# Optimization experiments

Measured on AMD Instinct MI355X. Metric: run time of the kernel, lower is better.

## Reference

```python
import jax, jax.numpy as jnp
import numpy as np

N = 20000      # nodes
E = 320000     # directed edges (before self-loops)
IN, HID, HEADS, OUT = 512, 256, 4, 256
NEG_SLOPE = 0.2  # PyG GATConv default


def setup_inputs() -> dict:
    key = jax.random.key(0)
    ks = jax.random.split(key, 10)
    x = jax.random.normal(ks[0], (N, IN), jnp.float32)
    edge_index = jax.random.randint(ks[1], (2, E), 0, N, jnp.int32)
    W1 = jax.random.normal(ks[2], (IN, HEADS * HID), jnp.float32) / np.sqrt(IN).astype(np.float32)
    att_src1 = jax.random.normal(ks[3], (HEADS, HID), jnp.float32) * 0.1
    att_dst1 = jax.random.normal(ks[4], (HEADS, HID), jnp.float32) * 0.1
    b1 = jnp.zeros((HEADS * HID,), jnp.float32)
    W2 = jax.random.normal(ks[5], (HEADS * HID, OUT), jnp.float32) / np.sqrt(HEADS * HID).astype(np.float32)
    att_src2 = jax.random.normal(ks[6], (1, OUT), jnp.float32) * 0.1
    att_dst2 = jax.random.normal(ks[7], (1, OUT), jnp.float32) * 0.1
    b2 = jnp.zeros((OUT,), jnp.float32)
    return {"x": x, "edge_index": edge_index, "W1": W1, "att_src1": att_src1,
            "att_dst1": att_dst1, "b1": b1, "W2": W2, "att_src2": att_src2,
            "att_dst2": att_dst2, "b2": b2}


def _segment_softmax(logits, seg, num_segments):
    # softmax over edges grouped by destination node (per head)
    m = jax.ops.segment_max(logits, seg, num_segments=num_segments)
    ex = jnp.exp(logits - m[seg])
    s = jax.ops.segment_sum(ex, seg, num_segments=num_segments)
    return ex / (s[seg] + 1e-16)


def _gat_conv(x, src, dst, W, att_src, att_dst, bias, heads, ch, num_nodes, concat):
    # PyG GATConv: h = W x (per head); alpha_e = softmax_dst(LeakyReLU(a_s.h_src + a_d.h_dst))
    h = (x @ W).reshape(num_nodes, heads, ch)          # [N,H,C]
    a_s = (h * att_src).sum(-1)                        # [N,H]
    a_d = (h * att_dst).sum(-1)                        # [N,H]
    logits = jax.nn.leaky_relu(a_s[src] + a_d[dst], NEG_SLOPE)   # [E,H]
    alpha = _segment_softmax(logits, dst, num_nodes)             # [E,H]
    msg = h[src] * alpha[:, :, None]                             # [E,H,C]
    out = jax.ops.segment_sum(msg, dst, num_segments=num_nodes)  # [N,H,C]
    out = out.reshape(num_nodes, heads * ch) if concat else out.mean(axis=1)
    return out + bias


def reference(x, edge_index, W1, att_src1, att_dst1, b1, W2, att_src2, att_dst2, b2):
    # add self-loops (PyG default add_self_loops=True)
    loop = jnp.arange(N, dtype=edge_index.dtype)
    src = jnp.concatenate([edge_index[0], loop])
    dst = jnp.concatenate([edge_index[1], loop])
    h = jax.nn.elu(_gat_conv(x, src, dst, W1, att_src1, att_dst1, b1, HEADS, HID, N, True))
    return _gat_conv(h, src, dst, W2, att_src2, att_dst2, b2, 1, OUT, N, False)
```

## Files before the change

### kernel.cpp

```cpp
#include <hip/hip_runtime.h>
#include <hip/hip_bf16.h>
#include <cfloat>
#include <math.h>

#define N_NODES 20000
#define M_PAD   20096
#define N_EDGES 320000
#define TOT_E   (N_EDGES + N_NODES)
#define IN_F    512
#define HID     256
#define HEADS   4
#define OUT_F   256
#define H1DIM   (HEADS * HID)
#define NEG_SLOPE 0.2f

typedef __attribute__((ext_vector_type(8))) __bf16 bf16x8;
typedef __attribute__((ext_vector_type(4))) __bf16 bf16x4;
typedef __attribute__((ext_vector_type(4))) float f32x4;

__device__ __forceinline__ float lrelu(float x) { return x >= 0.f ? x : NEG_SLOPE * x; }

__global__ void k_count(const int* __restrict__ ei, int* __restrict__ deg) {
  int e = blockIdx.x * 256 + threadIdx.x;
  if (e >= TOT_E) return;
  int dst = (e < N_EDGES) ? ei[N_EDGES + e] : (e - N_EDGES);
  atomicAdd(&deg[dst], 1);
}

__global__ void k_scan(const int* __restrict__ deg, int* __restrict__ off) {
  __shared__ int part[256];
  int tid = threadIdx.x;
  const int chunk = (N_NODES + 255) / 256;
  int s0 = tid * chunk;
  int s1 = s0 + chunk; if (s1 > N_NODES) s1 = N_NODES; if (s0 > N_NODES) s0 = N_NODES;
  int s = 0;
  for (int i = s0; i < s1; ++i) s += deg[i];
  part[tid] = s;
  __syncthreads();
  for (int d = 1; d < 256; d <<= 1) {
    int v = (tid >= d) ? part[tid - d] : 0;
    __syncthreads();
    part[tid] += v;
    __syncthreads();
  }
  int run = (tid == 0) ? 0 : part[tid - 1];
  for (int i = s0; i < s1; ++i) { off[i] = run; run += deg[i]; }
  if (tid == 255) off[N_NODES] = run;
}

__global__ void k_fill(const int* __restrict__ ei, const int* __restrict__ off,
                       int* __restrict__ cur, int* __restrict__ csr_src) {
  int e = blockIdx.x * 256 + threadIdx.x;
  if (e >= TOT_E) return;
  int src, dst;
  if (e < N_EDGES) { src = ei[e]; dst = ei[N_EDGES + e]; }
  else             { src = dst = e - N_EDGES; }
  int pos = atomicAdd(&cur[dst], 1);
  csr_src[off[dst] + pos] = src;
}

__global__ void k_f2b(const float* __restrict__ in, __bf16* __restrict__ out, int n4) {
  int i = blockIdx.x * 256 + threadIdx.x;
  if (i >= n4) return;
  float4 v = ((const float4*)in)[i];
  bf16x4 o = { (__bf16)v.x, (__bf16)v.y, (__bf16)v.z, (__bf16)v.w };
  ((bf16x4*)out)[i] = o;
}

__global__ void k_tr_f2b(const float* __restrict__ in, __bf16* __restrict__ out,
                         int R, int Cc) {
  __shared__ float tile[32][33];
  int c0 = blockIdx.x * 32, r0 = blockIdx.y * 32;
  int tx = threadIdx.x & 31, ty = threadIdx.x >> 5;
  for (int rr = ty; rr < 32; rr += 8)
    tile[rr][tx] = in[(size_t)(r0 + rr) * Cc + c0 + tx];
  __syncthreads();
  for (int rr = ty; rr < 32; rr += 8)
    out[(size_t)(c0 + rr) * R + r0 + tx] = (__bf16)tile[tx][rr];
}

__global__ __launch_bounds__(256) void k_gemm_bf16(
    const __bf16* __restrict__ A,
    const __bf16* __restrict__ Bt,
    __bf16* __restrict__ Cb,
    int M, int N, int K)
{
  __shared__ char lds[32768];
  char* As = lds;
  char* Bs = lds + 16384;

  const int t = threadIdx.x;
  const int lane = t & 63;
  const int wid = t >> 6;
  const int wm = wid >> 1, wn = wid & 1;
  const int row0 = blockIdx.y * 128;
  const int col0 = blockIdx.x * 128;

  f32x4 acc[4][4];
#pragma unroll
  for (int i = 0; i < 4; ++i)
#pragma unroll
    for (int j = 0; j < 4; ++j) acc[i][j] = (f32x4){0.f, 0.f, 0.f, 0.f};

  for (int k0 = 0; k0 < K; k0 += 64) {
#pragma unroll
    for (int i = 0; i < 4; ++i) {
      int j = i * 256 + t;
      int r = j >> 3;
      int cc = (j & 7) ^ (r & 7);
      const __bf16* gp = A + (size_t)(row0 + r) * K + k0 + cc * 8;
      __builtin_amdgcn_global_load_lds(
          (const __attribute__((address_space(1))) void*)gp,
          (__attribute__((address_space(3))) void*)(As + j * 16), 16, 0, 0);
    }
#pragma unroll
    for (int i = 0; i < 4; ++i) {
      int j = i * 256 + t;
      int r = j >> 3;
      int cc = (j & 7) ^ (r & 7);
      const __bf16* gp = Bt + (size_t)(col0 + r) * K + k0 + cc * 8;
      __builtin_amdgcn_global_load_lds(
          (const __attribute__((address_space(1))) void*)gp,
          (__attribute__((address_space(3))) void*)(Bs + j * 16), 16, 0, 0);
    }
    __syncthreads();

#pragma unroll
    for (int ks = 0; ks < 2; ++ks) {
      bf16x8 af[4], bfr[4];
#pragma unroll
      for (int i = 0; i < 4; ++i) {
        int rA = wm * 64 + i * 16 + (lane & 15);
        int chA = (ks * 4 + (lane >> 4)) ^ (rA & 7);
        af[i] = *(const bf16x8*)(As + rA * 128 + chA * 16);
        int rB = wn * 64 + i * 16 + (lane & 15);
        int chB = (ks * 4 + (lane >> 4)) ^ (rB & 7);
        bfr[i] = *(const bf16x8*)(Bs + rB * 128 + chB * 16);
      }
#pragma unroll
      for (int i = 0; i < 4; ++i)
#pragma unroll
        for (int jn = 0; jn < 4; ++jn)
          acc[i][jn] = __builtin_amdgcn_mfma_f32_16x16x32_bf16(
              af[i], bfr[jn], acc[i][jn], 0, 0, 0);
    }
    __syncthreads();
  }

#pragma unroll
  for (int i = 0; i < 4; ++i) {
    int growb = row0 + wm * 64 + i * 16 + (lane >> 4) * 4;
#pragma unroll
    for (int jn = 0; jn < 4; ++jn) {
      int gcol = col0 + wn * 64 + jn * 16 + (lane & 15);
#pragma unroll
      for (int r = 0; r < 4; ++r) {
        int grow = growb + r;
        if (grow < M) Cb[(size_t)grow * N + gcol] = (__bf16)acc[i][jn][r];
      }
    }
  }
}

__global__ void k_attn1(const __bf16* __restrict__ h1b, const float* __restrict__ att_s,
                        const float* __restrict__ att_d, float* __restrict__ as,
                        float* __restrict__ ad) {
  int n = blockIdx.x;
  int t = threadIdx.x;
  int head = t >> 6, lane = t & 63;
  bf16x4 hv = *(const bf16x4*)(h1b + (size_t)n * H1DIM + t * 4);
  float4 sv = *(const float4*)(att_s + t * 4);
  float4 dv = *(const float4*)(att_d + t * 4);
  float h0 = (float)hv[0], h1 = (float)hv[1], h2 = (float)hv[2], h3 = (float)hv[3];
  float ss = h0 * sv.x + h1 * sv.y + h2 * sv.z + h3 * sv.w;
  float sd = h0 * dv.x + h1 * dv.y + h2 * dv.z + h3 * dv.w;
#pragma unroll
  for (int d = 32; d; d >>= 1) { ss += __shfl_xor(ss, d); sd += __shfl_xor(sd, d); }
  if (lane == 0) { as[n * HEADS + head] = ss; ad[n * HEADS + head] = sd; }
}

__global__ void k_attn2(const __bf16* __restrict__ h2b, const float* __restrict__ att_s,
                        const float* __restrict__ att_d, float* __restrict__ as,
                        float* __restrict__ ad) {
  int n = blockIdx.x;
  int lane = threadIdx.x;
  bf16x4 hv = *(const bf16x4*)(h2b + (size_t)n * OUT_F + lane * 4);
  float4 sv = *(const float4*)(att_s + lane * 4);
  float4 dv = *(const float4*)(att_d + lane * 4);
  float h0 = (float)hv[0], h1 = (float)hv[1], h2 = (float)hv[2], h3 = (float)hv[3];
  float ss = h0 * sv.x + h1 * sv.y + h2 * sv.z + h3 * sv.w;
  float sd = h0 * dv.x + h1 * dv.y + h2 * dv.z + h3 * dv.w;
#pragma unroll
  for (int d = 32; d; d >>= 1) { ss += __shfl_xor(ss, d); sd += __shfl_xor(sd, d); }
  if (lane == 0) { as[n] = ss; ad[n] = sd; }
}

__global__ void k_w1(const int* __restrict__ off, const int* __restrict__ csr,
                     const float* __restrict__ as, const float* __restrict__ ad,
                     float* __restrict__ wn, float* __restrict__ inv) {
  int n = blockIdx.x;
  int lane = threadIdx.x;
  int beg = off[n], end = off[n + 1];
  float4 adv = *(const float4*)&ad[n * 4];
  float p0 = 0.f, p1 = 0.f, p2 = 0.f, p3 = 0.f;
  for (int p = beg + lane; p < end; p += 64) {
    int s = csr[p];
    float4 av = *(const float4*)&as[s * 4];
    float w0 = __expf(lrelu(av.x + adv.x));
    float w1 = __expf(lrelu(av.y + adv.y));
    float w2 = __expf(lrelu(av.z + adv.z));
    float w3 = __expf(lrelu(av.w + adv.w));
    p0 += w0; p1 += w1; p2 += w2; p3 += w3;
    float4 wv = {w0, w1, w2, w3};
    *(float4*)&wn[(size_t)p * 4] = wv;
  }
#pragma unroll
  for (int d = 32; d; d >>= 1) {
    p0 += __shfl_xor(p0, d); p1 += __shfl_xor(p1, d);
    p2 += __shfl_xor(p2, d); p3 += __shfl_xor(p3, d);
  }
  if (lane == 0) {
    float4 iv = {1.f / (p0 + 1e-16f), 1.f / (p1 + 1e-16f),
                 1.f / (p2 + 1e-16f), 1.f / (p3 + 1e-16f)};
    *(float4*)&inv[n * 4] = iv;
  }
}

__global__ void k_w2(const int* __restrict__ off, const int* __restrict__ csr,
                     const float* __restrict__ as, const float* __restrict__ ad,
                     float* __restrict__ wn, float* __restrict__ inv) {
  int n = blockIdx.x;
  int lane = threadIdx.x;
  int beg = off[n], end = off[n + 1];
  float adv = ad[n];
  float ps = 0.f;
  for (int p = beg + lane; p < end; p += 64) {
    int s = csr[p];
    float w = __expf(lrelu(as[s] + adv));
    wn[p] = w;
    ps += w;
  }
#pragma unroll
  for (int d = 32; d; d >>= 1) ps += __shfl_xor(ps, d);
  if (lane == 0) inv[n] = 1.f / (ps + 1e-16f);
}

__global__ __launch_bounds__(256) void k_gather1(
    const int* __restrict__ off, const int* __restrict__ csr,
    const __bf16* __restrict__ h1b, const float* __restrict__ wn,
    const float* __restrict__ inv, const float* __restrict__ b1,
    __bf16* __restrict__ heluB) {
  int bid = blockIdx.x;
  int slice = bid & 7;
  int grp = bid >> 3;
  int wid = threadIdx.x >> 6, lane = threadIdx.x & 63;
  int n = grp * 4 + wid;
  int cb = slice * 128;
  int head = slice >> 1;
  int sub = lane >> 4, cg = lane & 15;
  int beg = off[n], end = off[n + 1];

  float acc[8] = {0.f, 0.f, 0.f, 0.f, 0.f, 0.f, 0.f, 0.f};
  const __bf16* hb = h1b + cb + cg * 8;
#pragma unroll 2
  for (int p = beg; p < end; p += 4) {
    int e = p + sub;
    float w = 0.f; int s = 0;
    if (e < end) { s = csr[e]; w = wn[(size_t)e * 4 + head]; }
    bf16x8 hv = *(const bf16x8*)(hb + (size_t)s * H1DIM);
#pragma unroll
    for (int k = 0; k < 8; ++k) acc[k] += w * (float)hv[k];
  }
#pragma unroll
  for (int k = 0; k < 8; ++k) {
    acc[k] += __shfl_xor(acc[k], 16);
    acc[k] += __shfl_xor(acc[k], 32);
  }
  if (sub == 0) {
    float iv = inv[n * 4 + head];
    float4 b0 = *(const float4*)(b1 + cb + cg * 8);
    float4 b1v = *(const float4*)(b1 + cb + cg * 8 + 4);
    float bb[8] = {b0.x, b0.y, b0.z, b0.w, b1v.x, b1v.y, b1v.z, b1v.w};
    bf16x8 o;
#pragma unroll
    for (int k = 0; k < 8; ++k) {
      float v = acc[k] * iv + bb[k];
      v = v > 0.f ? v : expm1f(v);
      o[k] = (__bf16)v;
    }
    *(bf16x8*)(heluB + (size_t)n * H1DIM + cb + cg * 8) = o;
  }
}

__global__ __launch_bounds__(256) void k_gather2(
    const int* __restrict__ off, const int* __restrict__ csr,
    const __bf16* __restrict__ h2b, const float* __restrict__ wn,
    const float* __restrict__ inv, const float* __restrict__ b2,
    float* __restrict__ out) {
  int bid = blockIdx.x;
  int slice = bid & 3;
  int grp = bid >> 2;
  int wid = threadIdx.x >> 6, lane = threadIdx.x & 63;
  int n = grp * 4 + wid;
  int cb = slice * 64;
  int sub = lane >> 3, cg = lane & 7;
  int beg = off[n], end = off[n + 1];

  float acc[8] = {0.f, 0.f, 0.f, 0.f, 0.f, 0.f, 0.f, 0.f};
  const __bf16* hb = h2b + cb + cg * 8;
#pragma unroll 2
  for (int p = beg; p < end; p += 8) {
    int e = p + sub;
    float w = 0.f; int s = 0;
    if (e < end) { s = csr[e]; w = wn[e]; }
    bf16x8 hv = *(const bf16x8*)(hb + (size_t)s * OUT_F);
#pragma unroll
    for (int k = 0; k < 8; ++k) acc[k] += w * (float)hv[k];
  }
#pragma unroll
  for (int k = 0; k < 8; ++k) {
    acc[k] += __shfl_xor(acc[k], 8);
    acc[k] += __shfl_xor(acc[k], 16);
    acc[k] += __shfl_xor(acc[k], 32);
  }
  if (sub == 0) {
    float iv = inv[n];
    float4 b0 = *(const float4*)(b2 + cb + cg * 8);
    float4 b1v = *(const float4*)(b2 + cb + cg * 8 + 4);
    float* op = out + (size_t)n * OUT_F + cb + cg * 8;
    float4 o0 = {acc[0] * iv + b0.x, acc[1] * iv + b0.y,
                 acc[2] * iv + b0.z, acc[3] * iv + b0.w};
    float4 o1 = {acc[4] * iv + b1v.x, acc[5] * iv + b1v.y,
                 acc[6] * iv + b1v.z, acc[7] * iv + b1v.w};
    *(float4*)op = o0;
    *(float4*)(op + 4) = o1;
  }
}

extern "C" void kernel_launch(void* const* d_in, const int* in_sizes, int n_in,
                              void* d_out, int out_size, void* d_ws, size_t ws_size,
                              hipStream_t stream) {
  const float* x      = (const float*)d_in[0];
  const int*   ei     = (const int*)d_in[1];
  const float* W1     = (const float*)d_in[2];
  const float* att_s1 = (const float*)d_in[3];
  const float* att_d1 = (const float*)d_in[4];
  const float* b1     = (const float*)d_in[5];
  const float* W2     = (const float*)d_in[6];
  const float* att_s2 = (const float*)d_in[7];
  const float* att_d2 = (const float*)d_in[8];
  const float* b2     = (const float*)d_in[9];
  float* out = (float*)d_out;

  char* w = (char*)d_ws;
  auto alloc = [&](size_t bytes) {
    char* p = w;
    w += (bytes + 255) & ~(size_t)255;
    return p;
  };
  int*    deg   = (int*)alloc((size_t)N_NODES * 4);
  int*    off   = (int*)alloc((size_t)(N_NODES + 1) * 4);
  int*    cur   = (int*)alloc((size_t)N_NODES * 4);
  int*    csr   = (int*)alloc((size_t)TOT_E * 4);
  float*  as1   = (float*)alloc((size_t)N_NODES * HEADS * 4);
  float*  ad1   = (float*)alloc((size_t)N_NODES * HEADS * 4);
  float*  as2   = (float*)alloc((size_t)N_NODES * 4);
  float*  ad2   = (float*)alloc((size_t)N_NODES * 4);
  float*  wn1   = (float*)alloc((size_t)TOT_E * HEADS * 4);
  float*  inv1  = (float*)alloc((size_t)N_NODES * HEADS * 4);
  float*  wn2   = (float*)alloc((size_t)TOT_E * 4);
  float*  inv2  = (float*)alloc((size_t)N_NODES * 4);
  __bf16* xb    = (__bf16*)alloc((size_t)M_PAD * IN_F * 2);
  __bf16* w1t   = (__bf16*)alloc((size_t)H1DIM * IN_F * 2);
  __bf16* w2t   = (__bf16*)alloc((size_t)OUT_F * H1DIM * 2);
  __bf16* h1b   = (__bf16*)alloc((size_t)M_PAD * H1DIM * 2);
  __bf16* heluB = (__bf16*)alloc((size_t)M_PAD * H1DIM * 2);
  __bf16* h2b   = (__bf16*)alloc((size_t)M_PAD * OUT_F * 2);
  if ((size_t)(w - (char*)d_ws) > ws_size) return;

  hipMemsetAsync(deg, 0, (size_t)N_NODES * 4, stream);
  hipMemsetAsync(cur, 0, (size_t)N_NODES * 4, stream);

  k_count<<<(TOT_E + 255) / 256, 256, 0, stream>>>(ei, deg);
  k_scan<<<1, 256, 0, stream>>>(deg, off);
  k_fill<<<(TOT_E + 255) / 256, 256, 0, stream>>>(ei, off, cur, csr);

  int n4 = N_NODES * IN_F / 4;
  k_f2b<<<(n4 + 255) / 256, 256, 0, stream>>>(x, xb, n4);
  k_tr_f2b<<<dim3(H1DIM / 32, IN_F / 32), 256, 0, stream>>>(W1, w1t, IN_F, H1DIM);
  k_tr_f2b<<<dim3(OUT_F / 32, H1DIM / 32), 256, 0, stream>>>(W2, w2t, H1DIM, OUT_F);

  k_gemm_bf16<<<dim3(H1DIM / 128, M_PAD / 128), 256, 0, stream>>>(
      xb, w1t, h1b, N_NODES, H1DIM, IN_F);
  k_attn1<<<N_NODES, 256, 0, stream>>>(h1b, att_s1, att_d1, as1, ad1);
  k_w1<<<N_NODES, 64, 0, stream>>>(off, csr, as1, ad1, wn1, inv1);
  k_gather1<<<(N_NODES / 4) * 8, 256, 0, stream>>>(off, csr, h1b, wn1, inv1, b1, heluB);

  k_gemm_bf16<<<dim3(OUT_F / 128, M_PAD / 128), 256, 0, stream>>>(
      heluB, w2t, h2b, N_NODES, OUT_F, H1DIM);
  k_attn2<<<N_NODES, 64, 0, stream>>>(h2b, att_s2, att_d2, as2, ad2);
  k_w2<<<N_NODES, 64, 0, stream>>>(off, csr, as2, ad2, wn2, inv2);
  k_gather2<<<(N_NODES / 4) * 4, 256, 0, stream>>>(off, csr, h2b, wn2, inv2, b2, out);
}
```

Before: 324.0 us.

## Map multiple nodes per wave in gather kernels, drop cross-lane reductions

Both gather kernels now give each 16-lane (layer 1) or 8-lane (layer 2) lane group its own destination node. Each group walks that node's edges serially up to the wave's maximum degree, instead of splitting one node's edges across sub-groups and reducing with shuffles. This removes the shuffle reductions and the single-writer epilogue. It also uses bit-shift bf16 unpacking and a cheaper ELU. Edge arrays are padded and zeroed so overrun reads past the max-degree stay in bounds. The tradeoff is that lanes with small degree idle while the wave waits on its highest-degree node.

```diff
diff --git a/kernel.cpp b/kernel.cpp
--- a/kernel.cpp
+++ b/kernel.cpp
@@ -7,6 +7,7 @@
 #define M_PAD   20096
 #define N_EDGES 320000
 #define TOT_E   (N_EDGES + N_NODES)
+#define EPAD    512
 #define IN_F    512
 #define HID     256
 #define HEADS   4
@@ -19,6 +20,7 @@
 typedef __attribute__((ext_vector_type(4))) float f32x4;
 
 __device__ __forceinline__ float lrelu(float x) { return x >= 0.f ? x : NEG_SLOPE * x; }
+__device__ __forceinline__ float elu_lite(float x) { return x > 0.f ? x : __expf(x) - 1.f; }
 
 __global__ void k_count(const int* __restrict__ ei, int* __restrict__ deg) {
   int e = blockIdx.x * 256 + threadIdx.x;
@@ -252,44 +254,47 @@
     __bf16* __restrict__ heluB) {
   int bid = blockIdx.x;
   int slice = bid & 7;
-  int grp = bid >> 3;
-  int wid = threadIdx.x >> 6, lane = threadIdx.x & 63;
-  int n = grp * 4 + wid;
+  int head = slice >> 1;
   int cb = slice * 128;
-  int head = slice >> 1;
-  int sub = lane >> 4, cg = lane & 15;
+  int w = threadIdx.x >> 6, lane = threadIdx.x & 63;
+  int g = lane >> 4;
+  int cg = lane & 15;
+  int n = (bid >> 3) * 16 + w * 4 + g;
   int beg = off[n], end = off[n + 1];
+  int deg = end - beg;
+  int itmax = deg;
+  itmax = max(itmax, __shfl_xor(itmax, 16));
+  itmax = max(itmax, __shfl_xor(itmax, 32));
 
   float acc[8] = {0.f, 0.f, 0.f, 0.f, 0.f, 0.f, 0.f, 0.f};
   const __bf16* hb = h1b + cb + cg * 8;
 #pragma unroll 2
-  for (int p = beg; p < end; p += 4) {
-    int e = p + sub;
-    float w = 0.f; int s = 0;
-    if (e < end) { s = csr[e]; w = wn[(size_t)e * 4 + head]; }
-    bf16x8 hv = *(const bf16x8*)(hb + (size_t)s * H1DIM);
-#pragma unroll
-    for (int k = 0; k < 8; ++k) acc[k] += w * (float)hv[k];
-  }
+  for (int i = 0; i < itmax; ++i) {
+    int e = beg + i;
+    int s = csr[e];
+    float wv = (i < deg) ? wn[(size_t)e * 4 + head] : 0.f;
+    uint4 u = *(const uint4*)(hb + (size_t)s * H1DIM);
+    acc[0] = fmaf(wv, __uint_as_float(u.x << 16), acc[0]);
+    acc[1] = fmaf(wv, __uint_as_float(u.x & 0xffff0000u), acc[1]);
+    acc[2] = fmaf(wv, __uint_as_float(u.y << 16), acc[2]);
+    acc[3] = fmaf(wv, __uint_as_float(u.y & 0xffff0000u), acc[3]);
+    acc[4] = fmaf(wv, __uint_as_float(u.z << 16), acc[4]);
+    acc[5] = fmaf(wv, __uint_as_float(u.z & 0xffff0000u), acc[5]);
+    acc[6] = fmaf(wv, __uint_as_float(u.w << 16), acc[6]);
+    acc[7] = fmaf(wv, __uint_as_float(u.w & 0xffff0000u), acc[7]);
+  }
+
+  float iv = inv[n * 4 + head];
+  float4 bv0 = *(const float4*)(b1 + cb + cg * 8);
+  float4 bv1 = *(const float4*)(b1 + cb + cg * 8 + 4);
+  float bb[8] = {bv0.x, bv0.y, bv0.z, bv0.w, bv1.x, bv1.y, bv1.z, bv1.w};
+  bf16x8 o;
 #pragma unroll
   for (int k = 0; k < 8; ++k) {
-    acc[k] += __shfl_xor(acc[k], 16);
-    acc[k] += __shfl_xor(acc[k], 32);
-  }
-  if (sub == 0) {
-    float iv = inv[n * 4 + head];
-    float4 b0 = *(const float4*)(b1 + cb + cg * 8);
-    float4 b1v = *(const float4*)(b1 + cb + cg * 8 + 4);
-    float bb[8] = {b0.x, b0.y, b0.z, b0.w, b1v.x, b1v.y, b1v.z, b1v.w};
-    bf16x8 o;
-#pragma unroll
-    for (int k = 0; k < 8; ++k) {
-      float v = acc[k] * iv + bb[k];
-      v = v > 0.f ? v : expm1f(v);
-      o[k] = (__bf16)v;
-    }
-    *(bf16x8*)(heluB + (size_t)n * H1DIM + cb + cg * 8) = o;
-  }
+    float v = acc[k] * iv + bb[k];
+    o[k] = (__bf16)elu_lite(v);
+  }
+  *(bf16x8*)(heluB + (size_t)n * H1DIM + cb + cg * 8) = o;
 }
 
 __global__ __launch_bounds__(256) void k_gather2(
@@ -299,42 +304,46 @@
     float* __restrict__ out) {
   int bid = blockIdx.x;
   int slice = bid & 3;
-  int grp = bid >> 2;
-  int wid = threadIdx.x >> 6, lane = threadIdx.x & 63;
-  int n = grp * 4 + wid;
   int cb = slice * 64;
-  int sub = lane >> 3, cg = lane & 7;
+  int w = threadIdx.x >> 6, lane = threadIdx.x & 63;
+  int g = lane >> 3;
+  int cg = lane & 7;
+  int n = (bid >> 2) * 32 + w * 8 + g;
   int beg = off[n], end = off[n + 1];
+  int deg = end - beg;
+  int itmax = deg;
+  itmax = max(itmax, __shfl_xor(itmax, 8));
+  itmax = max(itmax, __shfl_xor(itmax, 16));
+  itmax = max(itmax, __shfl_xor(itmax, 32));
 
   float acc[8] = {0.f, 0.f, 0.f, 0.f, 0.f, 0.f, 0.f, 0.f};
   const __bf16* hb = h2b + cb + cg * 8;
 #pragma unroll 2
-  for (int p = beg; p < end; p += 8) {
-    int e = p + sub;
-    float w = 0.f; int s = 0;
-    if (e < end) { s = csr[e]; w = wn[e]; }
-    bf16x8 hv = *(const bf16x8*)(hb + (size_t)s * OUT_F);
-#pragma unroll
-    for (int k = 0; k < 8; ++k) acc[k] += w * (float)hv[k];
-  }
-#pragma unroll
-  for (int k = 0; k < 8; ++k) {
-    acc[k] += __shfl_xor(acc[k], 8);
-    acc[k] += __shfl_xor(acc[k], 16);
-    acc[k] += __shfl_xor(acc[k], 32);
-  }
-  if (sub == 0) {
-    float iv = inv[n];
-    float4 b0 = *(const float4*)(b2 + cb + cg * 8);
-    float4 b1v = *(const float4*)(b2 + cb + cg * 8 + 4);
-    float* op = out + (size_t)n * OUT_F + cb + cg * 8;
-    float4 o0 = {acc[0] * iv + b0.x, acc[1] * iv + b0.y,
-                 acc[2] * iv + b0.z, acc[3] * iv + b0.w};
-    float4 o1 = {acc[4] * iv + b1v.x, acc[5] * iv + b1v.y,
-                 acc[6] * iv + b1v.z, acc[7] * iv + b1v.w};
-    *(float4*)op = o0;
-    *(float4*)(op + 4) = o1;
-  }
+  for (int i = 0; i < itmax; ++i) {
+    int e = beg + i;
+    int s = csr[e];
+    float wv = (i < deg) ? wn[e] : 0.f;
+    uint4 u = *(const uint4*)(hb + (size_t)s * OUT_F);
+    acc[0] = fmaf(wv, __uint_as_float(u.x << 16), acc[0]);
+    acc[1] = fmaf(wv, __uint_as_float(u.x & 0xffff0000u), acc[1]);
+    acc[2] = fmaf(wv, __uint_as_float(u.y << 16), acc[2]);
+    acc[3] = fmaf(wv, __uint_as_float(u.y & 0xffff0000u), acc[3]);
+    acc[4] = fmaf(wv, __uint_as_float(u.z << 16), acc[4]);
+    acc[5] = fmaf(wv, __uint_as_float(u.z & 0xffff0000u), acc[5]);
+    acc[6] = fmaf(wv, __uint_as_float(u.w << 16), acc[6]);
+    acc[7] = fmaf(wv, __uint_as_float(u.w & 0xffff0000u), acc[7]);
+  }
+
+  float iv = inv[n];
+  float4 bv0 = *(const float4*)(b2 + cb + cg * 8);
+  float4 bv1 = *(const float4*)(b2 + cb + cg * 8 + 4);
+  float* op = out + (size_t)n * OUT_F + cb + cg * 8;
+  float4 o0 = {acc[0] * iv + bv0.x, acc[1] * iv + bv0.y,
+               acc[2] * iv + bv0.z, acc[3] * iv + bv0.w};
+  float4 o1 = {acc[4] * iv + bv1.x, acc[5] * iv + bv1.y,
+               acc[6] * iv + bv1.z, acc[7] * iv + bv1.w};
+  *(float4*)op = o0;
+  *(float4*)(op + 4) = o1;
 }
 
 extern "C" void kernel_launch(void* const* d_in, const int* in_sizes, int n_in,
@@ -361,14 +370,14 @@
   int*    deg   = (int*)alloc((size_t)N_NODES * 4);
   int*    off   = (int*)alloc((size_t)(N_NODES + 1) * 4);
   int*    cur   = (int*)alloc((size_t)N_NODES * 4);
-  int*    csr   = (int*)alloc((size_t)TOT_E * 4);
+  int*    csr   = (int*)alloc((size_t)(TOT_E + EPAD) * 4);
   float*  as1   = (float*)alloc((size_t)N_NODES * HEADS * 4);
   float*  ad1   = (float*)alloc((size_t)N_NODES * HEADS * 4);
   float*  as2   = (float*)alloc((size_t)N_NODES * 4);
   float*  ad2   = (float*)alloc((size_t)N_NODES * 4);
-  float*  wn1   = (float*)alloc((size_t)TOT_E * HEADS * 4);
+  float*  wn1   = (float*)alloc((size_t)(TOT_E + EPAD) * HEADS * 4);
   float*  inv1  = (float*)alloc((size_t)N_NODES * HEADS * 4);
-  float*  wn2   = (float*)alloc((size_t)TOT_E * 4);
+  float*  wn2   = (float*)alloc((size_t)(TOT_E + EPAD) * 4);
   float*  inv2  = (float*)alloc((size_t)N_NODES * 4);
   __bf16* xb    = (__bf16*)alloc((size_t)M_PAD * IN_F * 2);
   __bf16* w1t   = (__bf16*)alloc((size_t)H1DIM * IN_F * 2);
@@ -380,6 +389,7 @@
 
   hipMemsetAsync(deg, 0, (size_t)N_NODES * 4, stream);
   hipMemsetAsync(cur, 0, (size_t)N_NODES * 4, stream);
+  hipMemsetAsync(csr + TOT_E, 0, (size_t)EPAD * 4, stream);
 
   k_count<<<(TOT_E + 255) / 256, 256, 0, stream>>>(ei, deg);
   k_scan<<<1, 256, 0, stream>>>(deg, off);
@@ -394,11 +404,11 @@
       xb, w1t, h1b, N_NODES, H1DIM, IN_F);
   k_attn1<<<N_NODES, 256, 0, stream>>>(h1b, att_s1, att_d1, as1, ad1);
   k_w1<<<N_NODES, 64, 0, stream>>>(off, csr, as1, ad1, wn1, inv1);
-  k_gather1<<<(N_NODES / 4) * 8, 256, 0, stream>>>(off, csr, h1b, wn1, inv1, b1, heluB);
+  k_gather1<<<(N_NODES / 16) * 8, 256, 0, stream>>>(off, csr, h1b, wn1, inv1, b1, heluB);
 
   k_gemm_bf16<<<dim3(OUT_F / 128, M_PAD / 128), 256, 0, stream>>>(
       heluB, w2t, h2b, N_NODES, OUT_F, H1DIM);
   k_attn2<<<N_NODES, 64, 0, stream>>>(h2b, att_s2, att_d2, as2, ad2);
   k_w2<<<N_NODES, 64, 0, stream>>>(off, csr, as2, ad2, wn2, inv2);
-  k_gather2<<<(N_NODES / 4) * 4, 256, 0, stream>>>(off, csr, h2b, wn2, inv2, b2, out);
-}
+  k_gather2<<<(N_NODES / 32) * 4, 256, 0, stream>>>(off, csr, h2b, wn2, inv2, b2, out);
+}
```

New measurement: 307.3 us. 5.2% less time.
